# Performance work log

Measured on AMD Instinct MI355X. Metric: run time of the kernel, lower is better.

The kernel has to match this reference:

```python
import jax, jax.numpy as jnp
import numpy as np

P = 5          # config.num_pillars
H = 64         # config.hidden_dim // 4
B = 262144     # batch of pillar vectors
LN_EPS = 1e-5  # torch LayerNorm default eps
NORM_EPS = 1e-12  # F.normalize default eps


def _potential(x, W1, b1, W2, b2):
    # potential_net: Linear(P,H) -> GELU(exact) -> Linear(H,1)
    h = jax.nn.gelu(x @ W1 + b1, approximate=False)
    return h @ W2 + b2  # [..., 1]


def _layernorm(x, g, b):
    mu = x.mean(-1, keepdims=True)
    var = x.var(-1, keepdims=True)  # biased, matches torch LayerNorm
    return (x - mu) / jnp.sqrt(var + LN_EPS) * g + b


def setup_inputs() -> dict:
    key = jax.random.key(0)
    ks = jax.random.split(key, 8)
    s = lambda k, shape, scale: (jax.random.normal(k, shape, jnp.float32) * scale)
    return {
        "pillars": jax.random.uniform(ks[0], (B, P), jnp.float32),
        "W1": s(ks[1], (P, H), 1.0 / np.sqrt(P)),
        "b1": s(ks[2], (H,), 0.01),
        "W2": s(ks[3], (H, 1), 1.0 / np.sqrt(H)),
        "b2": s(ks[4], (1,), 0.01),
        "ln_gamma": jnp.ones((P,), jnp.float32),
        "ln_beta": jnp.zeros((P,), jnp.float32),
        "Wc": s(ks[5], (2 * P + 2, 1), 1.0 / np.sqrt(2 * P + 2)),
        "bc": s(ks[6], (1,), 0.01),
    }


def reference(pillars, W1, b1, W2, b2, ln_gamma, ln_beta, Wc, bc):
    # detect_catastrophe_batch path (includes compute_hessian_eigenvalues)
    p = jnp.clip(jnp.nan_to_num(pillars, nan=0.5), 0.0, 1.0)

    # V(p) and dV/dp  (batched; replaces per-call autograd.grad)
    V = _potential(p, W1, b1, W2, b2)  # [B,1]
    grad = jax.grad(lambda q: _potential(q, W1, b1, W2, b2).sum())(p)  # [B,P]

    # compute_hessian_eigenvalues: stabilize, per-sample 5x5 Hessian, eigvalsh
    x = _layernorm(p, ln_gamma, ln_beta)  # [B,P]
    pot_scalar = lambda xi: _potential(xi, W1, b1, W2, b2)[0]
    Hm = jax.vmap(jax.hessian(pot_scalar))(x)  # [B,P,P]
    Hm = 0.5 * (Hm + jnp.swapaxes(Hm, -1, -2))  # symmetrize (as in source)
    ev = jnp.linalg.eigvalsh(Hm)  # [B,P] ascending, matches torch.linalg.eigvalsh
    e_mean = ev.mean(-1, keepdims=True)  # [B,1]

    # features -> L2 normalize -> classifier -> clamp
    feats = jnp.concatenate([pillars, grad, V, e_mean], axis=-1)  # [B,2P+2]
    feats = feats / jnp.maximum(
        jnp.linalg.norm(feats, axis=-1, keepdims=True), NORM_EPS
    )
    probs = jnp.clip(jax.nn.sigmoid(feats @ Wc + bc), 0.0, 1.0)  # [B,1]
    return probs
```

## Files before the change

kernel.cpp:

```cpp
#include <hip/hip_runtime.h>
#include <math.h>

#define NP 5
#define NH 64
#define BLK 256

typedef float f32x2 __attribute__((ext_vector_type(2)));

#define LOG2E 1.44269504088896340736f
#define C_CDF0 2.30220840f
#define C_CDF1 0.10294324f
#define C_G2A 1.59576912f
#define C_G2B 0.21406460f
#define C_PDF_A (-0.72134752f)
#define C_PDF_B (-1.32574806f)

__global__ __launch_bounds__(BLK) void topo_kernel(
    const float* __restrict__ pillars,
    const float* __restrict__ gW1,
    const float* __restrict__ gb1,
    const float* __restrict__ gW2,
    const float* __restrict__ gb2,
    const float* __restrict__ gLng,
    const float* __restrict__ gLnb,
    const float* __restrict__ gWc,
    const float* __restrict__ gbc,
    float* __restrict__ out,
    int n)
{
    const int t = threadIdx.x;
    const long sidx = (long)blockIdx.x * BLK + t;
    if (sidx >= n) return;

    float gam[NP], bet[NP], wcf[12];
    #pragma unroll
    for (int j = 0; j < NP; ++j) { gam[j] = gLng[j]; bet[j] = gLnb[j]; }
    #pragma unroll
    for (int i = 0; i < 12; ++i) wcf[i] = gWc[i];
    const float b2v = gb2[0], bcv = gbc[0];

    const float* prow = pillars + sidx * NP;
    float raw[NP], p[NP], x[NP];
    #pragma unroll
    for (int j = 0; j < NP; ++j) raw[j] = prow[j];

    float mu = 0.f;
    #pragma unroll
    for (int j = 0; j < NP; ++j) {
        float v = raw[j];
        if (!(v == v)) v = 0.5f;
        v = fminf(fmaxf(v, 0.f), 1.f);
        p[j] = v; mu += v;
    }
    mu *= 0.2f;
    float var = 0.f;
    #pragma unroll
    for (int j = 0; j < NP; ++j) { float d = p[j] - mu; var += d * d; }
    var *= 0.2f;
    float inv = rsqrtf(var + 1e-5f);
    #pragma unroll
    for (int j = 0; j < NP; ++j) x[j] = (p[j] - mu) * inv * gam[j] + bet[j];

    f32x2 P[NP], X[NP];
    #pragma unroll
    for (int j = 0; j < NP; ++j) { P[j] = (f32x2){p[j], p[j]}; X[j] = (f32x2){x[j], x[j]}; }

    const f32x2 one = {1.f, 1.f}, two = {2.f, 2.f};
    const f32x2 cC0 = {-C_CDF0, -C_CDF0}, cC1 = {-C_CDF1, -C_CDF1};
    const f32x2 cGA = {C_G2A, C_G2A},     cGB = {C_G2B, C_G2B};
    const f32x2 cPA = {C_PDF_A, C_PDF_A}, cPB = {C_PDF_B, C_PDF_B};

    f32x2 V2 = {0.f,0.f}, TR = {0.f,0.f};
    f32x2 G0 = {0.f,0.f}, G1 = {0.f,0.f}, G2 = {0.f,0.f}, G3 = {0.f,0.f}, G4 = {0.f,0.f};

    #pragma unroll 4
    for (int pp = 0; pp < 32; ++pp) {
        const int k0 = 2 * pp;
        f32x2 w0 = {gW1[0*NH + k0], gW1[0*NH + k0 + 1]};
        f32x2 w1 = {gW1[1*NH + k0], gW1[1*NH + k0 + 1]};
        f32x2 w2 = {gW1[2*NH + k0], gW1[2*NH + k0 + 1]};
        f32x2 w3 = {gW1[3*NH + k0], gW1[3*NH + k0 + 1]};
        f32x2 w4 = {gW1[4*NH + k0], gW1[4*NH + k0 + 1]};
        f32x2 bb = {gb1[k0], gb1[k0 + 1]};
        f32x2 wo = {gW2[k0], gW2[k0 + 1]};

        f32x2 ssum = w0*w0 + (w1*w1 + (w2*w2 + (w3*w3 + w4*w4)));
        f32x2 sw = ssum * wo;

        f32x2 z  = P[0]*w0 + (P[1]*w1 + (P[2]*w2 + (P[3]*w3 + (P[4]*w4 + bb))));
        f32x2 zx = X[0]*w0 + (X[1]*w1 + (X[2]*w2 + (X[3]*w3 + (X[4]*w4 + bb))));

        f32x2 tz = z * z;
        f32x2 tx = zx * zx;

        f32x2 ya = z * (tz * cC1 + cC0);
        f32x2 e;
        e.x = __builtin_amdgcn_exp2f(ya.x);
        e.y = __builtin_amdgcn_exp2f(ya.y);
        f32x2 ope = e + one;
        f32x2 s;
        s.x = __builtin_amdgcn_rcpf(ope.x);
        s.y = __builtin_amdgcn_rcpf(ope.y);

        V2 = (z * s) * wo + V2;
        f32x2 u   = s - s * s;
        f32x2 g2p = tz * cGB + cGA;
        f32x2 d1  = ((z * u) * g2p + s) * wo;
        G0 = w0 * d1 + G0; G1 = w1 * d1 + G1; G2 = w2 * d1 + G2;
        G3 = w3 * d1 + G3; G4 = w4 * d1 + G4;

        f32x2 pa = tx * cPA + cPB;
        f32x2 ph;
        ph.x = __builtin_amdgcn_exp2f(pa.x);
        ph.y = __builtin_amdgcn_exp2f(pa.y);
        TR = (sw * (two - tx)) * ph + TR;
    }

    float V = V2.x + V2.y + b2v;
    float emean = 0.2f * (TR.x + TR.y);

    float f[12];
    f[0] = raw[0]; f[1] = raw[1]; f[2] = raw[2]; f[3] = raw[3]; f[4] = raw[4];
    f[5] = G0.x + G0.y; f[6] = G1.x + G1.y; f[7] = G2.x + G2.y;
    f[8] = G3.x + G3.y; f[9] = G4.x + G4.y;
    f[10] = V; f[11] = emean;

    float nrm = 0.f;
    #pragma unroll
    for (int i = 0; i < 12; ++i) nrm = fmaf(f[i], f[i], nrm);
    float denom = fmaxf(sqrtf(nrm), 1e-12f);
    float dot = 0.f;
    #pragma unroll
    for (int i = 0; i < 12; ++i) dot = fmaf(f[i], wcf[i], dot);
    float sarg = dot * __builtin_amdgcn_rcpf(denom) + bcv;
    float es = __builtin_amdgcn_exp2f(-sarg * LOG2E);
    float prob = __builtin_amdgcn_rcpf(1.0f + es);
    prob = fminf(fmaxf(prob, 0.f), 1.f);
    out[sidx] = prob;
}

extern "C" void kernel_launch(void* const* d_in, const int* in_sizes, int n_in,
                              void* d_out, int out_size, void* d_ws, size_t ws_size,
                              hipStream_t stream) {
    const float* pillars = (const float*)d_in[0];
    const float* W1  = (const float*)d_in[1];
    const float* b1  = (const float*)d_in[2];
    const float* W2  = (const float*)d_in[3];
    const float* b2  = (const float*)d_in[4];
    const float* lng = (const float*)d_in[5];
    const float* lnb = (const float*)d_in[6];
    const float* Wc  = (const float*)d_in[7];
    const float* bc  = (const float*)d_in[8];
    float* out = (float*)d_out;

    const int n = in_sizes[0] / NP;
    const int blocks = (n + BLK - 1) / BLK;
    topo_kernel<<<blocks, BLK, 0, stream>>>(
        pillars, W1, b1, W2, b2, lng, lnb, Wc, bc, out, n);
}
```

Before: 19.10 us.

## Split hidden dimension across two wavefronts per sample with LDS reduction

Each sample is now handled by two wavefronts, each covering half of the 64 hidden units, and the partial sums are combined through shared memory. This doubles the thread count and halves the serial per-thread loop, aiming to hide latency better and raise occupancy (launch bounds now request 8 blocks). In exchange, the per-sample prologue (load, clamp, LayerNorm) runs twice, and a __syncthreads plus an LDS round trip are added. FMA chains are also rebalanced into shorter trees to expose more instruction-level parallelism.

```diff
diff --git a/kernel.cpp b/kernel.cpp
--- a/kernel.cpp
+++ b/kernel.cpp
@@ -4,6 +4,7 @@
 #define NP 5
 #define NH 64
 #define BLK 256
+#define SPB 128
 
 typedef float f32x2 __attribute__((ext_vector_type(2)));
 
@@ -15,7 +16,7 @@
 #define C_PDF_A (-0.72134752f)
 #define C_PDF_B (-1.32574806f)
 
-__global__ __launch_bounds__(BLK) void topo_kernel(
+__global__ __launch_bounds__(BLK, 8) void topo_kernel(
     const float* __restrict__ pillars,
     const float* __restrict__ gW1,
     const float* __restrict__ gb1,
@@ -28,18 +29,23 @@
     float* __restrict__ out,
     int n)
 {
-    const int t = threadIdx.x;
-    const long sidx = (long)blockIdx.x * BLK + t;
-    if (sidx >= n) return;
+    __shared__ float sRed[SPB * 7];
 
-    float gam[NP], bet[NP], wcf[12];
+    const int t    = threadIdx.x;
+    const int lane = t & 63;
+    const int wid  = __builtin_amdgcn_readfirstlane(t >> 6);
+    const int half = wid & 1;
+    const int sgrp = wid >> 1;
+    const int sloc = sgrp * 64 + lane;
+    long sample = (long)blockIdx.x * SPB + sloc;
+    const bool valid = sample < n;
+    if (!valid) sample = n - 1;
+
+    float gam[NP], bet[NP];
     #pragma unroll
     for (int j = 0; j < NP; ++j) { gam[j] = gLng[j]; bet[j] = gLnb[j]; }
-    #pragma unroll
-    for (int i = 0; i < 12; ++i) wcf[i] = gWc[i];
-    const float b2v = gb2[0], bcv = gbc[0];
 
-    const float* prow = pillars + sidx * NP;
+    const float* prow = pillars + sample * NP;
     float raw[NP], p[NP], x[NP];
     #pragma unroll
     for (int j = 0; j < NP; ++j) raw[j] = prow[j];
@@ -73,22 +79,31 @@
     f32x2 V2 = {0.f,0.f}, TR = {0.f,0.f};
     f32x2 G0 = {0.f,0.f}, G1 = {0.f,0.f}, G2 = {0.f,0.f}, G3 = {0.f,0.f}, G4 = {0.f,0.f};
 
-    #pragma unroll 4
-    for (int pp = 0; pp < 32; ++pp) {
+    const int kb = half * 32;
+    const float* w0p = gW1 + 0*NH + kb;
+    const float* w1p = gW1 + 1*NH + kb;
+    const float* w2p = gW1 + 2*NH + kb;
+    const float* w3p = gW1 + 3*NH + kb;
+    const float* w4p = gW1 + 4*NH + kb;
+    const float* bbp = gb1 + kb;
+    const float* wop = gW2 + kb;
+
+    #pragma unroll 2
+    for (int pp = 0; pp < 16; ++pp) {
         const int k0 = 2 * pp;
-        f32x2 w0 = {gW1[0*NH + k0], gW1[0*NH + k0 + 1]};
-        f32x2 w1 = {gW1[1*NH + k0], gW1[1*NH + k0 + 1]};
-        f32x2 w2 = {gW1[2*NH + k0], gW1[2*NH + k0 + 1]};
-        f32x2 w3 = {gW1[3*NH + k0], gW1[3*NH + k0 + 1]};
-        f32x2 w4 = {gW1[4*NH + k0], gW1[4*NH + k0 + 1]};
-        f32x2 bb = {gb1[k0], gb1[k0 + 1]};
-        f32x2 wo = {gW2[k0], gW2[k0 + 1]};
+        f32x2 w0 = {w0p[k0], w0p[k0 + 1]};
+        f32x2 w1 = {w1p[k0], w1p[k0 + 1]};
+        f32x2 w2 = {w2p[k0], w2p[k0 + 1]};
+        f32x2 w3 = {w3p[k0], w3p[k0 + 1]};
+        f32x2 w4 = {w4p[k0], w4p[k0 + 1]};
+        f32x2 bb = {bbp[k0], bbp[k0 + 1]};
+        f32x2 wo = {wop[k0], wop[k0 + 1]};
 
-        f32x2 ssum = w0*w0 + (w1*w1 + (w2*w2 + (w3*w3 + w4*w4)));
+        f32x2 ssum = (w0*w0 + w1*w1) + (w2*w2 + w3*w3) + w4*w4;
         f32x2 sw = ssum * wo;
 
-        f32x2 z  = P[0]*w0 + (P[1]*w1 + (P[2]*w2 + (P[3]*w3 + (P[4]*w4 + bb))));
-        f32x2 zx = X[0]*w0 + (X[1]*w1 + (X[2]*w2 + (X[3]*w3 + (X[4]*w4 + bb))));
+        f32x2 z  = (P[0]*w0 + P[1]*w1) + (P[2]*w2 + P[3]*w3) + (P[4]*w4 + bb);
+        f32x2 zx = (X[0]*w0 + X[1]*w1) + (X[2]*w2 + X[3]*w3) + (X[4]*w4 + bb);
 
         f32x2 tz = z * z;
         f32x2 tx = zx * zx;
@@ -116,13 +131,35 @@
         TR = (sw * (two - tx)) * ph + TR;
     }
 
-    float V = V2.x + V2.y + b2v;
-    float emean = 0.2f * (TR.x + TR.y);
+    float pv = V2.x + V2.y;
+    float ptr = TR.x + TR.y;
+    float pg0 = G0.x + G0.y, pg1 = G1.x + G1.y, pg2 = G2.x + G2.y;
+    float pg3 = G3.x + G3.y, pg4 = G4.x + G4.y;
+
+    if (half) {
+        float* r = &sRed[sloc * 7];
+        r[0] = pv; r[1] = ptr; r[2] = pg0; r[3] = pg1; r[4] = pg2; r[5] = pg3; r[6] = pg4;
+    }
+    __syncthreads();
+    if (half) return;
+
+    {
+        const float* r = &sRed[sloc * 7];
+        pv  += r[0]; ptr += r[1];
+        pg0 += r[2]; pg1 += r[3]; pg2 += r[4]; pg3 += r[5]; pg4 += r[6];
+    }
+
+    float wcf[12];
+    #pragma unroll
+    for (int i = 0; i < 12; ++i) wcf[i] = gWc[i];
+    const float b2v = gb2[0], bcv = gbc[0];
+
+    float V = pv + b2v;
+    float emean = 0.2f * ptr;
 
     float f[12];
     f[0] = raw[0]; f[1] = raw[1]; f[2] = raw[2]; f[3] = raw[3]; f[4] = raw[4];
-    f[5] = G0.x + G0.y; f[6] = G1.x + G1.y; f[7] = G2.x + G2.y;
-    f[8] = G3.x + G3.y; f[9] = G4.x + G4.y;
+    f[5] = pg0; f[6] = pg1; f[7] = pg2; f[8] = pg3; f[9] = pg4;
     f[10] = V; f[11] = emean;
 
     float nrm = 0.f;
@@ -136,7 +173,7 @@
     float es = __builtin_amdgcn_exp2f(-sarg * LOG2E);
     float prob = __builtin_amdgcn_rcpf(1.0f + es);
     prob = fminf(fmaxf(prob, 0.f), 1.f);
-    out[sidx] = prob;
+    if (valid) out[sample] = prob;
 }
 
 extern "C" void kernel_launch(void* const* d_in, const int* in_sizes, int n_in,
@@ -154,7 +191,7 @@
     float* out = (float*)d_out;
 
     const int n = in_sizes[0] / NP;
-    const int blocks = (n + BLK - 1) / BLK;
+    const int blocks = (n + SPB - 1) / SPB;
     topo_kernel<<<blocks, BLK, 0, stream>>>(
         pillars, W1, b1, W2, b2, lng, lnb, Wc, bc, out, n);
 }
```

Result: slower. 21.21 us (+11.1%).
